# Optimization experiments

Measured on AMD Instinct MI355X. Metric: run time of the kernel, lower is better.

Reference implementation:

```python
import jax, jax.numpy as jnp
import numpy as np

ALPHA = 0.25


def setup_inputs() -> dict:
    key = jax.random.key(0)
    pos_seq = jax.random.normal(key, (64, 8192, 51), dtype=jnp.float32)
    return {"pos_seq": pos_seq}


def _ema(pos_seq, alpha):
    # out[0] = x[0]; out[t] = alpha*x[t] + (1-alpha)*out[t-1]
    x0 = pos_seq[:, 0]                      # (B, D)
    xs = jnp.swapaxes(pos_seq[:, 1:], 0, 1)  # (T-1, B, D) for scan over time

    def step(carry, x_t):
        y = alpha * x_t + (1.0 - alpha) * carry
        return y, y

    _, ys = jax.lax.scan(step, x0, xs)      # ys: (T-1, B, D)
    ys = jnp.swapaxes(ys, 0, 1)             # (B, T-1, D)
    return jnp.concatenate([pos_seq[:, :1], ys], axis=1)


def reference(pos_seq):
    return _ema(pos_seq, ALPHA)
```

## Files before the change

### kernel.cpp

```cpp
#include <hip/hip_runtime.h>


typedef float vfloat4 __attribute__((ext_vector_type(4)));

#define T_DIM 8192
#define C_DIM 51
#define L_ROWS 128
#define H_ROWS 48
#define TILE_ROWS (L_ROWS + H_ROWS)
#define TILE_ELEMS (TILE_ROWS * C_DIM)
#define OUT_ELEMS (L_ROWS * C_DIM)
#define SUB_LEN 32
#define NSUB 4
#define NCHUNK (T_DIM / L_ROWS)

__global__ __launch_bounds__(256, 4) void ema_kernel(const float* __restrict__ x,
                                                     float* __restrict__ y) {
    __shared__ float tile[TILE_ELEMS];

    const int tid = threadIdx.x;
    const int chunk = blockIdx.x % NCHUNK;
    const int b = blockIdx.x / NCHUNK;
    const size_t plane = (size_t)b * ((size_t)T_DIM * C_DIM);
    const int t0 = chunk * L_ROWS;
    const int start_f = (t0 - H_ROWS) * C_DIM;

    const float* __restrict__ xp = x + plane;

    if (chunk != 0) {
        for (int j = tid; j < TILE_ELEMS / 4; j += 256) {
            vfloat4 v = *(const vfloat4*)(xp + start_f + 4 * j);
            *(vfloat4*)(&tile[4 * j]) = v;
        }
    } else {
        for (int j = tid; j < TILE_ELEMS / 4; j += 256) {
            int e = start_f + 4 * j;
            if (e >= 0) {
                *(vfloat4*)(&tile[4 * j]) = *(const vfloat4*)(xp + e);
            } else {
                vfloat4 v;
#pragma unroll
                for (int k = 0; k < 4; ++k) {
                    int c = (e + k + H_ROWS * C_DIM) % C_DIM;
                    v[k] = xp[c];
                }
                *(vfloat4*)(&tile[4 * j]) = v;
            }
        }
    }
    __syncthreads();

    const int c = tid % C_DIM;
    const int sub = tid / C_DIM;
    const bool active = (tid < NSUB * C_DIM);
    float acc = 0.0f;
    if (active) {
        const int tr = sub * SUB_LEN;
        acc = tile[tr * C_DIM + c];
#pragma unroll
        for (int i = 1; i < H_ROWS; ++i)
            acc = fmaf(0.25f, tile[(tr + i) * C_DIM + c], 0.75f * acc);
    }
    __syncthreads();

    if (active) {
        const int base = (H_ROWS + sub * SUB_LEN) * C_DIM + c;
#pragma unroll
        for (int i = 0; i < SUB_LEN; ++i) {
            float xv = tile[base + i * C_DIM];
            acc = fmaf(0.25f, xv, 0.75f * acc);
            tile[base + i * C_DIM] = acc;
        }
    }
    __syncthreads();

    float* __restrict__ yp = y + plane + (size_t)t0 * C_DIM;
    for (int j = tid; j < OUT_ELEMS / 4; j += 256) {
        vfloat4 v = *(const vfloat4*)(&tile[H_ROWS * C_DIM + 4 * j]);
        __builtin_nontemporal_store(v, (vfloat4*)(yp + 4 * j));
    }
}

extern "C" void kernel_launch(void* const* d_in, const int* in_sizes, int n_in,
                              void* d_out, int out_size, void* d_ws, size_t ws_size,
                              hipStream_t stream) {
    const float* x = (const float*)d_in[0];
    float* y = (float*)d_out;

    int B = in_sizes[0] / (T_DIM * C_DIM);
    int grid = B * NCHUNK;
    ema_kernel<<<grid, 256, 0, stream>>>(x, y);
}
```

Before: 190.4 us.

## Replace shared-memory tiled EMA with per-thread register streaming scan

Drops the LDS tile and block syncs. Each thread now streams three channels of one batch over a 64-row chunk with a 48-row warm-up halo, prefetching two rows ahead in registers and storing directly to global memory. This removes shared-memory staging and barrier costs. In exchange it relatively increases halo re-reads, loses float4 vector and nontemporal stores, and lengthens the serial dependency chain per thread.

```diff
diff --git a/kernel.cpp b/kernel.cpp
--- a/kernel.cpp
+++ b/kernel.cpp
@@ -1,84 +1,87 @@
 #include <hip/hip_runtime.h>
 
 
-typedef float vfloat4 __attribute__((ext_vector_type(4)));
+typedef float vf2 __attribute__((ext_vector_type(2)));
 
 #define T_DIM 8192
 #define C_DIM 51
-#define L_ROWS 128
-#define H_ROWS 48
-#define TILE_ROWS (L_ROWS + H_ROWS)
-#define TILE_ELEMS (TILE_ROWS * C_DIM)
-#define OUT_ELEMS (L_ROWS * C_DIM)
-#define SUB_LEN 32
-#define NSUB 4
-#define NCHUNK (T_DIM / L_ROWS)
+#define B_DIM 64
+#define CHUNK 64
+#define HALO 48
+#define NCHUNK (T_DIM / CHUNK)
+#define TPR 17
+#define TPCH (B_DIM * TPR)
+#define BLOCK 64
 
-__global__ __launch_bounds__(256, 4) void ema_kernel(const float* __restrict__ x,
-                                                     float* __restrict__ y) {
-    __shared__ float tile[TILE_ELEMS];
+__device__ __forceinline__ void load12(const float* __restrict__ p,
+                                       float& v0, float& v1, float& v2) {
+    vf2 v;
+    __builtin_memcpy(&v, p, 8);
+    v0 = v[0];
+    v1 = v[1];
+    v2 = p[2];
+}
 
-    const int tid = threadIdx.x;
-    const int chunk = blockIdx.x % NCHUNK;
-    const int b = blockIdx.x / NCHUNK;
-    const size_t plane = (size_t)b * ((size_t)T_DIM * C_DIM);
-    const int t0 = chunk * L_ROWS;
-    const int start_f = (t0 - H_ROWS) * C_DIM;
+__device__ __forceinline__ void store12(float* __restrict__ p,
+                                        float v0, float v1, float v2) {
+    vf2 v;
+    v[0] = v0;
+    v[1] = v1;
+    __builtin_memcpy(p, &v, 8);
+    p[2] = v2;
+}
 
-    const float* __restrict__ xp = x + plane;
+__global__ __launch_bounds__(BLOCK) void ema_kernel(const float* __restrict__ x,
+                                                    float* __restrict__ y) {
+    const int gid = blockIdx.x * BLOCK + threadIdx.x;
+    const int chunk = gid / TPCH;
+    if (chunk >= NCHUNK) return;
+    const int r = gid - chunk * TPCH;
+    const int b = r / TPR;
+    const int j = r - b * TPR;
 
-    if (chunk != 0) {
-        for (int j = tid; j < TILE_ELEMS / 4; j += 256) {
-            vfloat4 v = *(const vfloat4*)(xp + start_f + 4 * j);
-            *(vfloat4*)(&tile[4 * j]) = v;
+    const size_t base = (size_t)b * ((size_t)T_DIM * C_DIM) + 3 * j;
+    const int t0 = chunk * CHUNK;
+    const int tend = t0 + CHUNK;
+    const int tstart = (chunk == 0) ? 0 : (t0 - HALO);
+    const int tloop = (chunk == 0) ? 0 : (tstart + 1);
+
+    const float* __restrict__ px = x + base + (size_t)tstart * C_DIM;
+    float* __restrict__ py = y + base + (size_t)t0 * C_DIM;
+
+    float a0, a1, a2;
+    load12(px, a0, a1, a2);
+    px += (size_t)(tloop - tstart) * C_DIM;
+
+    float x0a, x0b, x0c, x1a, x1b, x1c;
+    load12(px, x0a, x0b, x0c); px += C_DIM;
+    load12(px, x1a, x1b, x1c); px += C_DIM;
+
+    int t = tloop;
+#pragma unroll 2
+    for (; t < tend - 2; ++t) {
+        float x2a, x2b, x2c;
+        load12(px, x2a, x2b, x2c);
+        px += C_DIM;
+        a0 = fmaf(0.75f, a0, 0.25f * x0a);
+        a1 = fmaf(0.75f, a1, 0.25f * x0b);
+        a2 = fmaf(0.75f, a2, 0.25f * x0c);
+        if (t >= t0) {
+            store12(py, a0, a1, a2);
+            py += C_DIM;
         }
-    } else {
-        for (int j = tid; j < TILE_ELEMS / 4; j += 256) {
-            int e = start_f + 4 * j;
-            if (e >= 0) {
-                *(vfloat4*)(&tile[4 * j]) = *(const vfloat4*)(xp + e);
-            } else {
-                vfloat4 v;
-#pragma unroll
-                for (int k = 0; k < 4; ++k) {
-                    int c = (e + k + H_ROWS * C_DIM) % C_DIM;
-                    v[k] = xp[c];
-                }
-                *(vfloat4*)(&tile[4 * j]) = v;
-            }
-        }
+        x0a = x1a; x0b = x1b; x0c = x1c;
+        x1a = x2a; x1b = x2b; x1c = x2c;
     }
-    __syncthreads();
-
-    const int c = tid % C_DIM;
-    const int sub = tid / C_DIM;
-    const bool active = (tid < NSUB * C_DIM);
-    float acc = 0.0f;
-    if (active) {
-        const int tr = sub * SUB_LEN;
-        acc = tile[tr * C_DIM + c];
-#pragma unroll
-        for (int i = 1; i < H_ROWS; ++i)
-            acc = fmaf(0.25f, tile[(tr + i) * C_DIM + c], 0.75f * acc);
-    }
-    __syncthreads();
-
-    if (active) {
-        const int base = (H_ROWS + sub * SUB_LEN) * C_DIM + c;
-#pragma unroll
-        for (int i = 0; i < SUB_LEN; ++i) {
-            float xv = tile[base + i * C_DIM];
-            acc = fmaf(0.25f, xv, 0.75f * acc);
-            tile[base + i * C_DIM] = acc;
-        }
-    }
-    __syncthreads();
-
-    float* __restrict__ yp = y + plane + (size_t)t0 * C_DIM;
-    for (int j = tid; j < OUT_ELEMS / 4; j += 256) {
-        vfloat4 v = *(const vfloat4*)(&tile[H_ROWS * C_DIM + 4 * j]);
-        __builtin_nontemporal_store(v, (vfloat4*)(yp + 4 * j));
-    }
+    a0 = fmaf(0.75f, a0, 0.25f * x0a);
+    a1 = fmaf(0.75f, a1, 0.25f * x0b);
+    a2 = fmaf(0.75f, a2, 0.25f * x0c);
+    store12(py, a0, a1, a2);
+    py += C_DIM;
+    a0 = fmaf(0.75f, a0, 0.25f * x1a);
+    a1 = fmaf(0.75f, a1, 0.25f * x1b);
+    a2 = fmaf(0.75f, a2, 0.25f * x1c);
+    store12(py, a0, a1, a2);
 }
 
 extern "C" void kernel_launch(void* const* d_in, const int* in_sizes, int n_in,
@@ -88,6 +91,7 @@
     float* y = (float*)d_out;
 
     int B = in_sizes[0] / (T_DIM * C_DIM);
-    int grid = B * NCHUNK;
-    ema_kernel<<<grid, 256, 0, stream>>>(x, y);
+    int total_threads = B * TPR * NCHUNK;
+    int grid = (total_threads + BLOCK - 1) / BLOCK;
+    ema_kernel<<<grid, BLOCK, 0, stream>>>(x, y);
 }
```

Measured after the change: 227.5 us. 1.19x slower.
